# Kernel tuning notes

Hardware: AMD Instinct MI355X
Metric: run time of the kernel (lower is better)

Reference implementation:

```python
import jax, jax.numpy as jnp
import numpy as np


def setup_inputs() -> dict:
    key = jax.random.key(0)
    k1, k2 = jax.random.split(key)
    B, C, N = 2, 3, 16384
    in_pc = jax.random.normal(k1, (B, C, N), dtype=jnp.float32)
    target_pc = jax.random.normal(k2, (B, C, N), dtype=jnp.float32)
    return {"in_pc": in_pc, "target_pc": target_pc}


def reference(in_pc, target_pc):
    # [B,3,N] -> [B,N,3]
    pc1 = jnp.transpose(in_pc, (0, 2, 1))
    pc2 = jnp.transpose(target_pc, (0, 2, 1))
    sqr = (-2.0 * jnp.einsum('bnc,bmc->bnm', pc1, pc2)
           + jnp.sum(pc1 ** 2, -1)[:, :, None]
           + jnp.sum(pc2 ** 2, -1)[:, None, :])
    dist1 = jnp.min(sqr, axis=-1)  # [B,N] NN from pc1 to pc2
    dist2 = jnp.min(sqr, axis=1)   # [B,M] NN from pc2 to pc1
    m_dist = (dist1 + dist2) / 2.0  # requires N == M (as in original)
    return jnp.mean(m_dist)
```

## Files before the change

### kernel.cpp

```cpp
#include <hip/hip_runtime.h>

#define BLK 512
#define MT 32
#define IA 2
#define IB 512
#define TJQ 512
#define SJ 4

typedef __attribute__((ext_vector_type(8))) short short8;
typedef __attribute__((ext_vector_type(16))) float f32x16;

#define FORCE_V(x) asm volatile("" : "+v"(x))

__device__ __forceinline__ unsigned int fmap(float f) {
  unsigned int b = __float_as_uint(f);
  return (b & 0x80000000u) ? ~b : (b | 0x80000000u);
}
__device__ __forceinline__ float funmap(unsigned int u) {
  return __uint_as_float((u & 0x80000000u) ? (u ^ 0x80000000u) : ~u);
}
__device__ __forceinline__ unsigned short f2bf(float f) {
  unsigned int u = __float_as_uint(f);
  u += 0x7FFFu + ((u >> 16) & 1u);
  return (unsigned short)(u >> 16);
}
__device__ __forceinline__ float bf2f(unsigned short h) {
  return __uint_as_float(((unsigned int)h) << 16);
}
__device__ __forceinline__ unsigned int pk(unsigned short a, unsigned short b) {
  return (unsigned int)a | ((unsigned int)b << 16);
}

union FragU { uint4 u; short8 s; };

__global__ __launch_bounds__(BLK, 2) void cl_mfma(
    const float* __restrict__ A, const float* __restrict__ Bp,
    unsigned int* __restrict__ umin, int N, int jslice, int Bn) {
  __shared__ uint4 sA[2][IB];
  __shared__ uint4 sB[2][TJQ];
  __shared__ float sNP[IB];

  const int zi = blockIdx.z;
  const int dir = zi / Bn;
  const int b = zi - dir * Bn;
  const float* __restrict__ P = dir ? Bp : A;
  const float* __restrict__ Q = dir ? A : Bp;
  unsigned int* __restrict__ um = umin + ((size_t)dir * Bn + b) * N;

  const int t = threadIdx.x;
  const int ib0 = blockIdx.x * IB;
  const int jbase = blockIdx.y * jslice;
  const size_t boff = (size_t)b * 3 * N;
  const unsigned short one = 0x3F80u;

  {
    int i = ib0 + t;
    float x = P[boff + i], y = P[boff + N + i], zz = P[boff + 2 * N + i];
    float ax = -2.f * x, ay = -2.f * y, az = -2.f * zz;
    unsigned short hx = f2bf(ax), hy = f2bf(ay), hz = f2bf(az);
    unsigned short lx = f2bf(ax - bf2f(hx)), ly = f2bf(ay - bf2f(hy)),
                   lz = f2bf(az - bf2f(hz));
    sA[0][t] = make_uint4(pk(hx, hy), pk(hz, lx), pk(ly, lz), pk(hx, hy));
    sA[1][t] = make_uint4(pk(hz, lx), pk(ly, lz), pk(one, one), pk(one, 0));
    sNP[t] = fmaf(zz, zz, fmaf(y, y, x * x));
  }
  __syncthreads();

  const int w = t >> 6, l = t & 63, m = l & 31, g = l >> 5;
  FragU a0u, a1u;
  a0u.u = sA[g][w * (MT * IA) + m];
  a1u.u = sA[g][w * (MT * IA) + MT + m];
  const short8 af0 = a0u.s, af1 = a1u.s;

  float run0[16], run1[16];
  f32x16 zc;
#pragma unroll
  for (int r = 0; r < 16; ++r) { run0[r] = 3.0e38f; run1[r] = 3.0e38f; zc[r] = 0.0f; }
  FORCE_V(zc);

  const int nch = jslice / TJQ;
  float qx = Q[boff + jbase + t];
  float qy = Q[boff + N + jbase + t];
  float qz = Q[boff + 2 * N + jbase + t];

  for (int ch = 0; ch < nch; ++ch) {
    unsigned short hx = f2bf(qx), hy = f2bf(qy), hz = f2bf(qz);
    unsigned short lx = f2bf(qx - bf2f(hx)), ly = f2bf(qy - bf2f(hy)),
                   lz = f2bf(qz - bf2f(hz));
    float nq = fmaf(qz, qz, fmaf(qy, qy, qx * qx));
    unsigned short nh = f2bf(nq);
    float r1 = nq - bf2f(nh);
    unsigned short nm = f2bf(r1);
    unsigned short nl = f2bf(r1 - bf2f(nm));
    uint4 b0s = make_uint4(pk(hx, hy), pk(hz, hx), pk(hy, hz), pk(lx, ly));
    uint4 b1s = make_uint4(pk(lz, lx), pk(ly, lz), pk(nh, nm), pk(nl, 0));

    __syncthreads();
    sB[0][t] = b0s;
    sB[1][t] = b1s;
    {
      int jn = (ch + 1 < nch) ? (jbase + (ch + 1) * TJQ + t) : (jbase + t);
      qx = Q[boff + jn];
      qy = Q[boff + N + jn];
      qz = Q[boff + 2 * N + jn];
    }
    __syncthreads();

#pragma unroll
    for (int jt = 0; jt < TJQ / MT; jt += 2) {
      FragU ba, bb;
      ba.u = sB[g][(jt + 0) * MT + m];
      bb.u = sB[g][(jt + 1) * MT + m];
      f32x16 d0 = __builtin_amdgcn_mfma_f32_32x32x16_bf16(af0, ba.s, zc, 0, 0, 0);
      f32x16 d1 = __builtin_amdgcn_mfma_f32_32x32x16_bf16(af0, bb.s, zc, 0, 0, 0);
      FORCE_V(d0); FORCE_V(d1);
#pragma unroll
      for (int r = 0; r < 16; ++r)
        run0[r] = fminf(fminf(run0[r], d0[r]), d1[r]);
      f32x16 d2 = __builtin_amdgcn_mfma_f32_32x32x16_bf16(af1, ba.s, zc, 0, 0, 0);
      f32x16 d3 = __builtin_amdgcn_mfma_f32_32x32x16_bf16(af1, bb.s, zc, 0, 0, 0);
      FORCE_V(d2); FORCE_V(d3);
#pragma unroll
      for (int r = 0; r < 16; ++r)
        run1[r] = fminf(fminf(run1[r], d2[r]), d3[r]);
    }
  }

#pragma unroll
  for (int r = 0; r < 16; ++r) {
    float v0 = run0[r], v1 = run1[r];
#pragma unroll
    for (int sh = 1; sh <= 16; sh <<= 1) {
      v0 = fminf(v0, __shfl_xor(v0, sh));
      v1 = fminf(v1, __shfl_xor(v1, sh));
    }
    if (m == 0) {
      int row = (r & 3) + 8 * (r >> 2) + 4 * g;
      int il0 = w * (MT * IA) + row;
      int il1 = il0 + MT;
      atomicMin(&um[ib0 + il0], fmap(v0 + sNP[il0]));
      atomicMin(&um[ib0 + il1], fmap(v1 + sNP[il1]));
    }
  }
}

__global__ __launch_bounds__(256) void cl_reduce(
    const unsigned int* __restrict__ u, float* __restrict__ out, int total) {
  const int t = threadIdx.x;
  const uint4* __restrict__ u4 = (const uint4*)u;
  const int n4 = total / 4;
  const int gid = blockIdx.x * 256 + t;
  const int gstride = gridDim.x * 256;
  double s = 0.0;
  for (int i = gid; i < n4; i += gstride) {
    uint4 v = u4[i];
    s += (double)funmap(v.x) + (double)funmap(v.y) +
         (double)funmap(v.z) + (double)funmap(v.w);
  }
  for (int off = 32; off > 0; off >>= 1) s += __shfl_down(s, off, 64);
  __shared__ double sw[4];
  if ((t & 63) == 0) sw[t >> 6] = s;
  __syncthreads();
  if (t == 0) {
    double tot = sw[0] + sw[1] + sw[2] + sw[3];
    atomicAdd(out, (float)(tot / (double)total));
  }
}

extern "C" void kernel_launch(void* const* d_in, const int* in_sizes, int n_in,
                              void* d_out, int out_size, void* d_ws, size_t ws_size,
                              hipStream_t stream) {
  const float* in_pc = (const float*)d_in[0];
  const float* tgt_pc = (const float*)d_in[1];
  const int B = 2, N = 16384;
  unsigned int* u = (unsigned int*)d_ws;
  float* out = (float*)d_out;

  hipMemsetAsync(u, 0xFF, (size_t)2 * B * N * sizeof(unsigned int), stream);
  hipMemsetAsync(out, 0, sizeof(float), stream);

  const int jslice = N / SJ;
  dim3 grid(N / IB, SJ, 2 * B);
  cl_mfma<<<grid, dim3(BLK), 0, stream>>>(in_pc, tgt_pc, u, N, jslice, B);

  const int total = 2 * B * N;
  cl_reduce<<<dim3(16), dim3(256), 0, stream>>>(u, out, total);
}
```

Before: 99.66 us.

## Double-buffer query tiles in LDS and software-pipeline fragment loads and MFMAs

Query tiles now sit in a two-stage LDS buffer. The next chunk is converted and stored while the current one is consumed, which cuts the two barriers per chunk down to one. Inside the inner loop the next B fragments are prefetched from LDS ahead of the MFMAs, and all four MFMAs are issued before the min reductions so they overlap better. This costs twice the LDS for sB and more live registers (64 extra accumulator values plus prefetched fragments), which may hurt occupancy under the 2-block launch bound.

Measured after the change: 100.3 us. Within noise of the previous version (+0.6%).

```diff
diff --git a/kernel.cpp b/kernel.cpp
--- a/kernel.cpp
+++ b/kernel.cpp
@@ -33,11 +33,25 @@
 
 union FragU { uint4 u; short8 s; };
 
+__device__ __forceinline__ void conv_q(float qx, float qy, float qz,
+                                       uint4& b0s, uint4& b1s) {
+  unsigned short hx = f2bf(qx), hy = f2bf(qy), hz = f2bf(qz);
+  unsigned short lx = f2bf(qx - bf2f(hx)), ly = f2bf(qy - bf2f(hy)),
+                 lz = f2bf(qz - bf2f(hz));
+  float nq = fmaf(qz, qz, fmaf(qy, qy, qx * qx));
+  unsigned short nh = f2bf(nq);
+  float r1 = nq - bf2f(nh);
+  unsigned short nm = f2bf(r1);
+  unsigned short nl = f2bf(r1 - bf2f(nm));
+  b0s = make_uint4(pk(hx, hy), pk(hz, hx), pk(hy, hz), pk(lx, ly));
+  b1s = make_uint4(pk(lz, lx), pk(ly, lz), pk(nh, nm), pk(nl, 0));
+}
+
 __global__ __launch_bounds__(BLK, 2) void cl_mfma(
     const float* __restrict__ A, const float* __restrict__ Bp,
     unsigned int* __restrict__ umin, int N, int jslice, int Bn) {
   __shared__ uint4 sA[2][IB];
-  __shared__ uint4 sB[2][TJQ];
+  __shared__ uint4 sB[2][2][TJQ];
   __shared__ float sNP[IB];
 
   const int zi = blockIdx.z;
@@ -64,6 +78,23 @@
     sA[1][t] = make_uint4(pk(hz, lx), pk(ly, lz), pk(one, one), pk(one, 0));
     sNP[t] = fmaf(zz, zz, fmaf(y, y, x * x));
   }
+
+  const int nch = jslice / TJQ;
+  float qx = Q[boff + jbase + t];
+  float qy = Q[boff + N + jbase + t];
+  float qz = Q[boff + 2 * N + jbase + t];
+  {
+    uint4 b0s, b1s;
+    conv_q(qx, qy, qz, b0s, b1s);
+    sB[0][0][t] = b0s;
+    sB[0][1][t] = b1s;
+  }
+  {
+    int j1 = jbase + (nch > 1 ? TJQ : 0) + t;
+    qx = Q[boff + j1];
+    qy = Q[boff + N + j1];
+    qz = Q[boff + 2 * N + j1];
+  }
   __syncthreads();
 
   const int w = t >> 6, l = t & 63, m = l & 31, g = l >> 5;
@@ -78,52 +109,43 @@
   for (int r = 0; r < 16; ++r) { run0[r] = 3.0e38f; run1[r] = 3.0e38f; zc[r] = 0.0f; }
   FORCE_V(zc);
 
-  const int nch = jslice / TJQ;
-  float qx = Q[boff + jbase + t];
-  float qy = Q[boff + N + jbase + t];
-  float qz = Q[boff + 2 * N + jbase + t];
-
   for (int ch = 0; ch < nch; ++ch) {
-    unsigned short hx = f2bf(qx), hy = f2bf(qy), hz = f2bf(qz);
-    unsigned short lx = f2bf(qx - bf2f(hx)), ly = f2bf(qy - bf2f(hy)),
-                   lz = f2bf(qz - bf2f(hz));
-    float nq = fmaf(qz, qz, fmaf(qy, qy, qx * qx));
-    unsigned short nh = f2bf(nq);
-    float r1 = nq - bf2f(nh);
-    unsigned short nm = f2bf(r1);
-    unsigned short nl = f2bf(r1 - bf2f(nm));
-    uint4 b0s = make_uint4(pk(hx, hy), pk(hz, hx), pk(hy, hz), pk(lx, ly));
-    uint4 b1s = make_uint4(pk(lz, lx), pk(ly, lz), pk(nh, nm), pk(nl, 0));
-
-    __syncthreads();
-    sB[0][t] = b0s;
-    sB[1][t] = b1s;
-    {
-      int jn = (ch + 1 < nch) ? (jbase + (ch + 1) * TJQ + t) : (jbase + t);
+    const int cur = ch & 1;
+    if (ch + 1 < nch) {
+      uint4 b0s, b1s;
+      conv_q(qx, qy, qz, b0s, b1s);
+      sB[cur ^ 1][0][t] = b0s;
+      sB[cur ^ 1][1][t] = b1s;
+      int jn = jbase + ((ch + 2 < nch) ? (ch + 2) : (ch + 1)) * TJQ + t;
       qx = Q[boff + jn];
       qy = Q[boff + N + jn];
       qz = Q[boff + 2 * N + jn];
     }
-    __syncthreads();
-
+
+    FragU ba, bb, bna, bnb;
+    ba.u = sB[cur][g][m];
+    bb.u = sB[cur][g][MT + m];
 #pragma unroll
     for (int jt = 0; jt < TJQ / MT; jt += 2) {
-      FragU ba, bb;
-      ba.u = sB[g][(jt + 0) * MT + m];
-      bb.u = sB[g][(jt + 1) * MT + m];
+      if (jt + 2 < TJQ / MT) {
+        bna.u = sB[cur][g][(jt + 2) * MT + m];
+        bnb.u = sB[cur][g][(jt + 3) * MT + m];
+      }
       f32x16 d0 = __builtin_amdgcn_mfma_f32_32x32x16_bf16(af0, ba.s, zc, 0, 0, 0);
       f32x16 d1 = __builtin_amdgcn_mfma_f32_32x32x16_bf16(af0, bb.s, zc, 0, 0, 0);
-      FORCE_V(d0); FORCE_V(d1);
+      f32x16 d2 = __builtin_amdgcn_mfma_f32_32x32x16_bf16(af1, ba.s, zc, 0, 0, 0);
+      f32x16 d3 = __builtin_amdgcn_mfma_f32_32x32x16_bf16(af1, bb.s, zc, 0, 0, 0);
+      FORCE_V(d0); FORCE_V(d1); FORCE_V(d2); FORCE_V(d3);
 #pragma unroll
       for (int r = 0; r < 16; ++r)
         run0[r] = fminf(fminf(run0[r], d0[r]), d1[r]);
-      f32x16 d2 = __builtin_amdgcn_mfma_f32_32x32x16_bf16(af1, ba.s, zc, 0, 0, 0);
-      f32x16 d3 = __builtin_amdgcn_mfma_f32_32x32x16_bf16(af1, bb.s, zc, 0, 0, 0);
-      FORCE_V(d2); FORCE_V(d3);
 #pragma unroll
       for (int r = 0; r < 16; ++r)
         run1[r] = fminf(fminf(run1[r], d2[r]), d3[r]);
-    }
+      ba = bna;
+      bb = bnb;
+    }
+    __syncthreads();
   }
 
 #pragma unroll
```
